# Performance work log

Hardware: AMD Instinct MI355X
Metric: run time of the kernel (lower is better)

## Reference

```python
import jax, jax.numpy as jnp
import numpy as np

NODES = 23   # 22 players + ball per frame-graph
K = 8        # random neighbors per node
B, T = 64, 128
G = B * T            # total graphs (frames)
N = G * NODES        # total nodes
D_IN, H, RH = 16, 128, 128


def setup_inputs() -> dict:
    key = jax.random.key(0)
    ks = jax.random.split(key, 10)
    x = jax.random.normal(ks[0], (N, D_IN), jnp.float32)
    # per-graph random edges: dst = each node repeated K times, src = random node in same graph
    src_local = jax.random.randint(ks[1], (G, NODES * K), 0, NODES)
    dst_local = jnp.tile(jnp.repeat(jnp.arange(NODES), K)[None, :], (G, 1))
    off = (jnp.arange(G) * NODES)[:, None]
    edge_index = jnp.stack([(src_local + off).reshape(-1),
                            (dst_local + off).reshape(-1)]).astype(jnp.int32)
    runner_idx = jax.random.randint(ks[2], (G,), 0, NODES, dtype=jnp.int32)
    sc = lambda k, sh: (jax.random.normal(k, sh, jnp.float32) * 0.05)
    return {
        'x': x, 'edge_index': edge_index, 'runner_idx': runner_idx,
        'W1': sc(ks[3], (D_IN, H)), 'b1': jnp.zeros((H,), jnp.float32),
        'W2': sc(ks[4], (H, H)),    'b2': jnp.zeros((H,), jnp.float32),
        'W_ih': sc(ks[5], (3 * RH, H)), 'W_hh': sc(ks[6], (3 * RH, RH)),
        'b_ih': jnp.zeros((3 * RH,), jnp.float32), 'b_hh': jnp.zeros((3 * RH,), jnp.float32),
        'Wp': sc(ks[7], (RH, 2)), 'bp': jnp.zeros((2,), jnp.float32),
    }


def _gcn_conv(h, edge_index, W, b):
    # PyG GCNConv: add self-loops, symmetric normalization, scatter-sum
    h = h @ W
    loop = jnp.arange(N, dtype=edge_index.dtype)
    s = jnp.concatenate([edge_index[0], loop])
    d = jnp.concatenate([edge_index[1], loop])
    deg = jax.ops.segment_sum(jnp.ones_like(s, h.dtype), d, num_segments=N)
    dinv = jnp.where(deg > 0, jax.lax.rsqrt(deg), 0.0)
    norm = dinv[s] * dinv[d]                      # [E+N]
    out = jax.ops.segment_sum(h[s] * norm[:, None], d, num_segments=N)
    return out + b


def _gru(seq, W_ih, W_hh, b_ih, b_hh):
    # torch GRU: gates in r,z,n order
    xg = seq @ W_ih.T + b_ih                      # [B,T,3RH]
    def step(hprev, xt):
        gh = hprev @ W_hh.T + b_hh
        xr, xz, xn = jnp.split(xt, 3, axis=-1)
        hr, hz, hn = jnp.split(gh, 3, axis=-1)
        r = jax.nn.sigmoid(xr + hr)
        z = jax.nn.sigmoid(xz + hz)
        n = jnp.tanh(xn + r * hn)
        hnew = (1.0 - z) * n + z * hprev
        return hnew, hnew
    h0 = jnp.zeros((seq.shape[0], RH), seq.dtype)
    _, outs = jax.lax.scan(step, h0, jnp.swapaxes(xg, 0, 1))
    return jnp.swapaxes(outs, 0, 1)               # [B,T,RH]


def reference(x, edge_index, runner_idx, W1, b1, W2, b2,
              W_ih, W_hh, b_ih, b_hh, Wp, bp):
    h = jax.nn.relu(_gcn_conv(x, edge_index, W1, b1))
    h = jax.nn.relu(_gcn_conv(h, edge_index, W2, b2))
    # fused equivalent of the per-graph nonzero()/indexing loop:
    runner_global = jnp.arange(G, dtype=jnp.int32) * NODES + runner_idx
    seq = h[runner_global].reshape(B, T, H)       # all lengths == T, padding is a no-op
    out = _gru(seq, W_ih, W_hh, b_ih, b_hh)
    return out @ Wp + bp                          # [B,T,2]
```

## Files before the change

### kernel.cpp

```cpp
#include <hip/hip_runtime.h>
#include <hip/hip_bf16.h>
#include <math.h>

#define GG 8192
#define NODESN 23
#define KK 8
#define DIN 16
#define HH 128
#define RHH 128
#define EPG (NODESN*KK)
#define TTT 128
#define BBB 64

template<int CTRL>
static __device__ __forceinline__ float dpp_add(float v) {
    int x = __builtin_amdgcn_update_dpp(0, __float_as_int(v), CTRL, 0xF, 0xF, true);
    return v + __int_as_float(x);
}
#define DPP_XOR1 0xB1
#define DPP_XOR2 0x4E
#define DPP_SHL4 0x104

__global__ __launch_bounds__(256) void gcn_hsum(
    const float* __restrict__ x, const int* __restrict__ esrc,
    const int* __restrict__ runner,
    const float* __restrict__ W1, const float* __restrict__ b1,
    float* __restrict__ xg )
{
    __shared__ float xs[NODESN * DIN];
    __shared__ int   srcs[EPG];
    __shared__ float t1[NODESN * HH];
    __shared__ float red[256];

    const int g   = blockIdx.x;
    const int tid = threadIdx.x;
    const int j   = tid & 127;
    const int nh  = tid >> 7;

    for (int i = tid; i < NODESN * DIN; i += 256) xs[i] = x[g * NODESN * DIN + i];
    for (int i = tid; i < EPG; i += 256)          srcs[i] = esrc[g * EPG + i] - g * NODESN;

    float w[DIN];
    #pragma unroll
    for (int k = 0; k < DIN; k++) w[k] = W1[k * HH + j];
    const float b1j = b1[j];
    __syncthreads();

    const int n0 = nh * 12;
    const int n1 = nh ? NODESN : 12;
    for (int n = n0; n < n1; n++) {
        float acc = 0.f;
        #pragma unroll
        for (int k = 0; k < DIN; k += 4) {
            float4 xv = *(const float4*)&xs[n * DIN + k];
            acc = fmaf(xv.x, w[k], fmaf(xv.y, w[k+1], fmaf(xv.z, w[k+2], fmaf(xv.w, w[k+3], acc))));
        }
        t1[n * HH + j] = acc;
    }
    __syncthreads();

    const int r = runner[g];
    float part = 0.f;
    for (int slot = nh; slot < 9; slot += 2) {
        int node = (slot < 8) ? srcs[r * KK + slot] : r;
        float acc = t1[node * HH + j];
        #pragma unroll
        for (int k = 0; k < KK; k++) acc += t1[srcs[node * KK + k] * HH + j];
        part += fmaxf(acc * (1.f / 9.f) + b1j, 0.f);
    }
    red[tid] = part;
    __syncthreads();
    if (tid < HH) xg[(size_t)g * 384 + tid] = red[tid] + red[tid + 128];
}

__global__ void pack_wih(const float* __restrict__ W, float* __restrict__ WTp)
{
    int idx = blockIdx.x * 256 + threadIdx.x;
    if (idx < 3 * RHH * RHH) {
        int j = idx / RHH, k = idx - j * RHH;
        WTp[(k >> 2) * (384 * 4) + j * 4 + (k & 3)] = W[idx];
    }
}

__global__ __launch_bounds__(384) void seqxg_kernel(
    float* __restrict__ xg, const float* __restrict__ W2,
    const float* __restrict__ b2, const float* __restrict__ WTp,
    const float* __restrict__ b_ih)
{
    __shared__ float hsb[16 * HH];
    __shared__ float sqb[16 * HH];
    const int tid = threadIdx.x;
    const size_t row0 = (size_t)blockIdx.x * 16;

    for (int v = tid; v < 16 * 32; v += 384) {
        int m = v >> 5, e = v & 31;
        ((float4*)hsb)[m * 32 + e] = *(const float4*)&xg[(row0 + m) * 384 + e * 4];
    }
    __syncthreads();

    {
        const int j = tid & 127, m0 = tid >> 7;
        const int nm = (m0 == 0) ? 6 : 5;
        float acc[6];
        #pragma unroll
        for (int t = 0; t < 6; t++) acc[t] = 0.f;
        for (int k = 0; k < HH; k += 4) {
            float w0 = W2[(k+0)*HH + j];
            float w1 = W2[(k+1)*HH + j];
            float w2 = W2[(k+2)*HH + j];
            float w3 = W2[(k+3)*HH + j];
            #pragma unroll
            for (int t = 0; t < 6; t++) {
                if (t < nm) {
                    float4 hv = *(const float4*)&hsb[(m0 + 3*t) * HH + k];
                    acc[t] = fmaf(hv.x, w0, fmaf(hv.y, w1, fmaf(hv.z, w2, fmaf(hv.w, w3, acc[t]))));
                }
            }
        }
        const float bj = b2[j];
        for (int t = 0; t < nm; t++)
            sqb[(m0 + 3*t) * HH + j] = fmaxf(acc[t] * (1.f/9.f) + bj, 0.f);
    }
    __syncthreads();

    {
        const int j2 = tid;
        float acc[16];
        const float bv = b_ih[j2];
        #pragma unroll
        for (int m = 0; m < 16; m++) acc[m] = bv;
        for (int k4 = 0; k4 < 32; k4++) {
            float4 wv = *(const float4*)&WTp[k4 * (384*4) + j2 * 4];
            #pragma unroll
            for (int m = 0; m < 16; m++) {
                float4 hv = *(const float4*)&sqb[m * HH + k4 * 4];
                acc[m] = fmaf(hv.x, wv.x, fmaf(hv.y, wv.y, fmaf(hv.z, wv.z, fmaf(hv.w, wv.w, acc[m]))));
            }
        }
        #pragma unroll
        for (int m = 0; m < 16; m++)
            xg[(row0 + m) * 384 + j2] = acc[m];
    }
}

#define CHUNK 32
#define NCH (TTT / CHUNK)
#define HPAD 132
#define XGB_FLOATS (CHUNK * HH * 4)

__global__ __launch_bounds__(512)
__attribute__((amdgpu_waves_per_eu(2, 2)))
void gru_kernel(
    const float* __restrict__ xg, const float* __restrict__ W_hh,
    const float* __restrict__ b_hh, const float* __restrict__ Wp,
    const float* __restrict__ bp, float* __restrict__ out)
{
    __shared__ float xgbuf[XGB_FLOATS];
    __shared__ float houtb[(CHUNK + 2) * HPAD];
    __shared__ float wps[2 * RHH + 2];

    const int b   = blockIdx.x;
    const int tid = threadIdx.x;
    const int q   = tid & 7;
    const int g   = tid >> 3;
    const int i0  = 2 * g, i1 = 2 * g + 1;

    float4 wr0[4], wz0[4], wn0[4], wr1[4], wz1[4], wn1[4];
    int lof[4];
    {
        const float* r0 = W_hh + (size_t)i0 * RHH;
        const float* z0 = r0 + (size_t)RHH * RHH;
        const float* n0 = z0 + (size_t)RHH * RHH;
        const float* r1 = W_hh + (size_t)i1 * RHH;
        const float* z1 = r1 + (size_t)RHH * RHH;
        const float* n1 = z1 + (size_t)RHH * RHH;
        #pragma unroll
        for (int m = 0; m < 4; m++) {
            int o = q * 16 + 4 * ((m + q) & 3);
            lof[m] = o;
            wr0[m] = *(const float4*)(r0 + o);
            wz0[m] = *(const float4*)(z0 + o);
            wn0[m] = *(const float4*)(n0 + o);
            wr1[m] = *(const float4*)(r1 + o);
            wz1[m] = *(const float4*)(z1 + o);
            wn1[m] = *(const float4*)(n1 + o);
        }
    }
    const float bhr0 = b_hh[i0], bhz0 = b_hh[RHH + i0], bhn0 = b_hh[2 * RHH + i0];
    const float bhr1 = b_hh[i1], bhz1 = b_hh[RHH + i1], bhn1 = b_hh[2 * RHH + i1];

    if (tid < 2 * RHH) wps[tid] = Wp[tid];
    if (tid < 2)       wps[2 * RHH + tid] = bp[tid];
    if (tid < HH)      houtb[CHUNK * HPAD + tid] = 0.f;
    float hp0 = 0.f, hp1 = 0.f;

    const float* xbase = xg + (size_t)b * TTT * 3 * RHH;
    float* outb = out + (size_t)b * TTT * 2;

    float pxr[8], pxz[8], pxn[8];
    #pragma unroll
    for (int k = 0; k < 8; k++) {
        int slot = tid + (k << 9);
        int tl = slot >> 7, ii = slot & 127;
        const float* p = xbase + (size_t)tl * 384 + ii;
        pxr[k] = p[0]; pxz[k] = p[128]; pxn[k] = p[256];
    }
    __syncthreads();

    for (int c = 0; c < NCH; c++) {
        #pragma unroll
        for (int k = 0; k < 8; k++) {
            int slot = tid + (k << 9);
            int tl = slot >> 7, ii = slot & 127;
            float4 v; v.x = pxr[k]; v.y = pxz[k]; v.z = pxn[k]; v.w = 0.f;
            *(float4*)&xgbuf[(tl << 9) + (ii << 2)] = v;
        }
        if (c + 1 < NCH) {
            #pragma unroll
            for (int k = 0; k < 8; k++) {
                int slot = tid + (k << 9);
                int tl = slot >> 7, ii = slot & 127;
                const float* p = xbase + (size_t)((c + 1) * CHUNK + tl) * 384 + ii;
                pxr[k] = p[0]; pxz[k] = p[128]; pxn[k] = p[256];
            }
        }
        if (c > 0) {
            const int s  = tid & 7;
            const int cc = (tid >> 3) & 1;
            const int tl = tid >> 4;
            const float* hr = &houtb[(tl + 1) * HPAD + s * 16];
            float acc = 0.f;
            #pragma unroll
            for (int jj = 0; jj < 4; jj++) {
                int mm = ((jj + s) & 3) << 2;
                float4 hv = *(const float4*)(hr + mm);
                int k = s * 16 + mm;
                acc = fmaf(hv.x, wps[(k+0)*2 + cc],
                      fmaf(hv.y, wps[(k+1)*2 + cc],
                      fmaf(hv.z, wps[(k+2)*2 + cc],
                      fmaf(hv.w, wps[(k+3)*2 + cc], acc))));
            }
            acc = dpp_add<DPP_XOR1>(acc);
            acc = dpp_add<DPP_XOR2>(acc);
            acc = dpp_add<DPP_SHL4>(acc);
            if (s == 0)
                outb[((c - 1) * CHUNK + tl) * 2 + cc] = acc + wps[2 * RHH + cc];
        }
        __syncthreads();

        for (int tl = 0; tl < CHUNK; tl++) {
            const float* hrow = &houtb[(tl == 0 ? CHUNK : tl) * HPAD];
            float ar0 = 0.f, az0 = 0.f, an0 = 0.f, ar1 = 0.f, az1 = 0.f, an1 = 0.f;
            #pragma unroll
            for (int m = 0; m < 4; m++) {
                float4 hv = *(const float4*)(hrow + lof[m]);
                ar0 = fmaf(hv.x, wr0[m].x, fmaf(hv.y, wr0[m].y, fmaf(hv.z, wr0[m].z, fmaf(hv.w, wr0[m].w, ar0))));
                az0 = fmaf(hv.x, wz0[m].x, fmaf(hv.y, wz0[m].y, fmaf(hv.z, wz0[m].z, fmaf(hv.w, wz0[m].w, az0))));
                an0 = fmaf(hv.x, wn0[m].x, fmaf(hv.y, wn0[m].y, fmaf(hv.z, wn0[m].z, fmaf(hv.w, wn0[m].w, an0))));
                ar1 = fmaf(hv.x, wr1[m].x, fmaf(hv.y, wr1[m].y, fmaf(hv.z, wr1[m].z, fmaf(hv.w, wr1[m].w, ar1))));
                az1 = fmaf(hv.x, wz1[m].x, fmaf(hv.y, wz1[m].y, fmaf(hv.z, wz1[m].z, fmaf(hv.w, wz1[m].w, az1))));
                an1 = fmaf(hv.x, wn1[m].x, fmaf(hv.y, wn1[m].y, fmaf(hv.z, wn1[m].z, fmaf(hv.w, wn1[m].w, an1))));
            }
            float4 x0 = *(const float4*)&xgbuf[(tl << 9) + (i0 << 2)];
            float4 x1 = *(const float4*)&xgbuf[(tl << 9) + (i1 << 2)];

            ar0 = dpp_add<DPP_XOR1>(ar0); ar0 = dpp_add<DPP_XOR2>(ar0); ar0 = dpp_add<DPP_SHL4>(ar0);
            az0 = dpp_add<DPP_XOR1>(az0); az0 = dpp_add<DPP_XOR2>(az0); az0 = dpp_add<DPP_SHL4>(az0);
            an0 = dpp_add<DPP_XOR1>(an0); an0 = dpp_add<DPP_XOR2>(an0); an0 = dpp_add<DPP_SHL4>(an0);
            ar1 = dpp_add<DPP_XOR1>(ar1); ar1 = dpp_add<DPP_XOR2>(ar1); ar1 = dpp_add<DPP_SHL4>(ar1);
            az1 = dpp_add<DPP_XOR1>(az1); az1 = dpp_add<DPP_XOR2>(az1); az1 = dpp_add<DPP_SHL4>(az1);
            an1 = dpp_add<DPP_XOR1>(an1); an1 = dpp_add<DPP_XOR2>(an1); an1 = dpp_add<DPP_SHL4>(an1);

            {
                float sr = x0.x + ar0 + bhr0;
                float sz = x0.y + az0 + bhz0;
                float rg = 1.f / (1.f + __expf(-sr));
                float zg = 1.f / (1.f + __expf(-sz));
                float tv = fmaf(rg, an0 + bhn0, x0.z);
                tv = fminf(fmaxf(tv, -15.f), 15.f);
                float e2 = __expf(-2.f * tv);
                float ng = (1.f - e2) / (1.f + e2);
                hp0 = fmaf(zg, hp0, (1.f - zg) * ng);
            }
            {
                float sr = x1.x + ar1 + bhr1;
                float sz = x1.y + az1 + bhz1;
                float rg = 1.f / (1.f + __expf(-sr));
                float zg = 1.f / (1.f + __expf(-sz));
                float tv = fmaf(rg, an1 + bhn1, x1.z);
                tv = fminf(fmaxf(tv, -15.f), 15.f);
                float e2 = __expf(-2.f * tv);
                float ng = (1.f - e2) / (1.f + e2);
                hp1 = fmaf(zg, hp1, (1.f - zg) * ng);
            }
            if (q == 0) {
                float2 hw; hw.x = hp0; hw.y = hp1;
                *(float2*)&houtb[(tl + 1) * HPAD + i0] = hw;
            }
            __syncthreads();
        }
    }

    {
        const int s  = tid & 7;
        const int cc = (tid >> 3) & 1;
        const int tl = tid >> 4;
        const float* hr = &houtb[(tl + 1) * HPAD + s * 16];
        float acc = 0.f;
        #pragma unroll
        for (int jj = 0; jj < 4; jj++) {
            int mm = ((jj + s) & 3) << 2;
            float4 hv = *(const float4*)(hr + mm);
            int k = s * 16 + mm;
            acc = fmaf(hv.x, wps[(k+0)*2 + cc],
                  fmaf(hv.y, wps[(k+1)*2 + cc],
                  fmaf(hv.z, wps[(k+2)*2 + cc],
                  fmaf(hv.w, wps[(k+3)*2 + cc], acc))));
        }
        acc = dpp_add<DPP_XOR1>(acc);
        acc = dpp_add<DPP_XOR2>(acc);
        acc = dpp_add<DPP_SHL4>(acc);
        if (s == 0)
            outb[((NCH - 1) * CHUNK + tl) * 2 + cc] = acc + wps[2 * RHH + cc];
    }
}

extern "C" void kernel_launch(void* const* d_in, const int* in_sizes, int n_in,
                              void* d_out, int out_size, void* d_ws, size_t ws_size,
                              hipStream_t stream)
{
    const float* x      = (const float*)d_in[0];
    const int*   eidx   = (const int*)d_in[1];
    const int*   runner = (const int*)d_in[2];
    const float* W1     = (const float*)d_in[3];
    const float* b1     = (const float*)d_in[4];
    const float* W2     = (const float*)d_in[5];
    const float* b2     = (const float*)d_in[6];
    const float* W_ih   = (const float*)d_in[7];
    const float* W_hh   = (const float*)d_in[8];
    const float* b_ih   = (const float*)d_in[9];
    const float* b_hh   = (const float*)d_in[10];
    const float* Wp     = (const float*)d_in[11];
    const float* bp     = (const float*)d_in[12];
    float* out = (float*)d_out;

    float* xg  = (float*)d_ws;
    float* WTp = xg + (size_t)GG * 3 * RHH;

    pack_wih<<<192, 256, 0, stream>>>(W_ih, WTp);
    gcn_hsum<<<GG, 256, 0, stream>>>(x, eidx, runner, W1, b1, xg);
    seqxg_kernel<<<GG / 16, 384, 0, stream>>>(xg, W2, b2, WTp, b_ih);
    gru_kernel<<<BBB, 512, 0, stream>>>(xg, W_hh, b_hh, Wp, bp, out);
}
```

Baseline: 256.9 us.

## Restructure GRU recurrence to one hidden unit per 4-lane group with packed FMA

The GRU kernel now assigns one hidden unit to each group of 4 lanes, where before it assigned two units to each group of 8. Each lane holds 96 weights as float2 vectors, so the matvec can use packed dual-FMA and needs only two DPP reduction steps instead of three. The register prefetch of the next xg chunk is dropped, so each chunk is loaded from global memory directly before the barrier. This adds global load latency on the serial path, and the wider per-lane weight set raises register pressure.

```diff
diff --git a/kernel.cpp b/kernel.cpp
--- a/kernel.cpp
+++ b/kernel.cpp
@@ -12,6 +12,8 @@
 #define TTT 128
 #define BBB 64
 
+typedef float v2f __attribute__((ext_vector_type(2)));
+
 template<int CTRL>
 static __device__ __forceinline__ float dpp_add(float v) {
     int x = __builtin_amdgcn_update_dpp(0, __float_as_int(v), CTRL, 0xF, 0xF, true);
@@ -19,13 +21,12 @@
 }
 #define DPP_XOR1 0xB1
 #define DPP_XOR2 0x4E
-#define DPP_SHL4 0x104
 
 __global__ __launch_bounds__(256) void gcn_hsum(
     const float* __restrict__ x, const int* __restrict__ esrc,
     const int* __restrict__ runner,
     const float* __restrict__ W1, const float* __restrict__ b1,
-    float* __restrict__ xg )
+    float* __restrict__ xg)
 {
     __shared__ float xs[NODESN * DIN];
     __shared__ int   srcs[EPG];
@@ -156,85 +157,135 @@
     const float* __restrict__ bp, float* __restrict__ out)
 {
     __shared__ float xgbuf[XGB_FLOATS];
-    __shared__ float houtb[(CHUNK + 2) * HPAD];
+    __shared__ float houtb[(CHUNK + 1) * HPAD];
     __shared__ float wps[2 * RHH + 2];
 
     const int b   = blockIdx.x;
     const int tid = threadIdx.x;
-    const int q   = tid & 7;
-    const int g   = tid >> 3;
-    const int i0  = 2 * g, i1 = 2 * g + 1;
-
-    float4 wr0[4], wz0[4], wn0[4], wr1[4], wz1[4], wn1[4];
-    int lof[4];
+    const int q   = tid & 3;
+    const int i   = tid >> 2;
+
+    v2f wr2[16], wz2[16], wn2[16];
+    int lof[8];
     {
-        const float* r0 = W_hh + (size_t)i0 * RHH;
-        const float* z0 = r0 + (size_t)RHH * RHH;
-        const float* n0 = z0 + (size_t)RHH * RHH;
-        const float* r1 = W_hh + (size_t)i1 * RHH;
-        const float* z1 = r1 + (size_t)RHH * RHH;
-        const float* n1 = z1 + (size_t)RHH * RHH;
-        #pragma unroll
-        for (int m = 0; m < 4; m++) {
-            int o = q * 16 + 4 * ((m + q) & 3);
-            lof[m] = o;
-            wr0[m] = *(const float4*)(r0 + o);
-            wz0[m] = *(const float4*)(z0 + o);
-            wn0[m] = *(const float4*)(n0 + o);
-            wr1[m] = *(const float4*)(r1 + o);
-            wz1[m] = *(const float4*)(z1 + o);
-            wn1[m] = *(const float4*)(n1 + o);
-        }
-    }
-    const float bhr0 = b_hh[i0], bhz0 = b_hh[RHH + i0], bhn0 = b_hh[2 * RHH + i0];
-    const float bhr1 = b_hh[i1], bhz1 = b_hh[RHH + i1], bhn1 = b_hh[2 * RHH + i1];
+        const float* br = W_hh + (size_t)i * RHH + q * 32;
+        const float* bz = br + (size_t)RHH * RHH;
+        const float* bn = bz + (size_t)RHH * RHH;
+        #pragma unroll
+        for (int m = 0; m < 8; m++) {
+            int p = (m + 2 * q) & 7;
+            lof[m] = q * 32 + 4 * p;
+            float4 v;
+            v = *(const float4*)(br + 4*p); wr2[2*m] = (v2f){v.x, v.y}; wr2[2*m+1] = (v2f){v.z, v.w};
+            v = *(const float4*)(bz + 4*p); wz2[2*m] = (v2f){v.x, v.y}; wz2[2*m+1] = (v2f){v.z, v.w};
+            v = *(const float4*)(bn + 4*p); wn2[2*m] = (v2f){v.x, v.y}; wn2[2*m+1] = (v2f){v.z, v.w};
+        }
+    }
+    const float bhr = b_hh[i];
+    const float bhz = b_hh[RHH + i];
+    const float bhn = b_hh[2 * RHH + i];
 
     if (tid < 2 * RHH) wps[tid] = Wp[tid];
     if (tid < 2)       wps[2 * RHH + tid] = bp[tid];
-    if (tid < HH)      houtb[CHUNK * HPAD + tid] = 0.f;
-    float hp0 = 0.f, hp1 = 0.f;
+    if (tid < HH)      houtb[tid] = 0.f;
+    float hprev = 0.f;
 
     const float* xbase = xg + (size_t)b * TTT * 3 * RHH;
     float* outb = out + (size_t)b * TTT * 2;
 
-    float pxr[8], pxz[8], pxn[8];
-    #pragma unroll
-    for (int k = 0; k < 8; k++) {
-        int slot = tid + (k << 9);
-        int tl = slot >> 7, ii = slot & 127;
-        const float* p = xbase + (size_t)tl * 384 + ii;
-        pxr[k] = p[0]; pxz[k] = p[128]; pxn[k] = p[256];
-    }
-    __syncthreads();
-
     for (int c = 0; c < NCH; c++) {
         #pragma unroll
-        for (int k = 0; k < 8; k++) {
-            int slot = tid + (k << 9);
+        for (int k2 = 0; k2 < 8; k2++) {
+            int slot = tid + (k2 << 9);
             int tl = slot >> 7, ii = slot & 127;
-            float4 v; v.x = pxr[k]; v.y = pxz[k]; v.z = pxn[k]; v.w = 0.f;
-            *(float4*)&xgbuf[(tl << 9) + (ii << 2)] = v;
-        }
-        if (c + 1 < NCH) {
+            const float* gsrc = xbase + (size_t)(c * CHUNK + tl) * 384 + ii;
+            float4 v;
+            v.x = gsrc[0]; v.y = gsrc[128]; v.z = gsrc[256]; v.w = 0.f;
+            *(float4*)&xgbuf[slot << 2] = v;
+        }
+        if (c > 0) {
+            const int s  = tid & 3;
+            const int cc = (tid >> 2) & 1;
+            const int tl = tid >> 3;
+            if (tl < CHUNK) {
+                const float* hr = &houtb[(tl + 1) * HPAD + s * 32];
+                float acc = 0.f;
+                #pragma unroll
+                for (int jj = 0; jj < 8; jj++) {
+                    int mm = 4 * ((jj + 2 * s) & 7);
+                    float4 hv = *(const float4*)(hr + mm);
+                    int k = s * 32 + mm;
+                    acc = fmaf(hv.x, wps[(k+0)*2 + cc],
+                          fmaf(hv.y, wps[(k+1)*2 + cc],
+                          fmaf(hv.z, wps[(k+2)*2 + cc],
+                          fmaf(hv.w, wps[(k+3)*2 + cc], acc))));
+                }
+                acc = dpp_add<DPP_XOR1>(acc);
+                acc = dpp_add<DPP_XOR2>(acc);
+                if (s == 0)
+                    outb[((c - 1) * CHUNK + tl) * 2 + cc] = acc + wps[2 * RHH + cc];
+            }
+        }
+        __syncthreads();
+
+        for (int tl = 0; tl < CHUNK; tl++) {
+            const float* hrow = &houtb[tl * HPAD];
+            float4 xgv = *(const float4*)&xgbuf[(tl * HH + i) << 2];
+            v2f arA = (v2f){0.f, 0.f}, arB = arA, azA = arA, azB = arA, anA = arA, anB = arA;
             #pragma unroll
-            for (int k = 0; k < 8; k++) {
-                int slot = tid + (k << 9);
-                int tl = slot >> 7, ii = slot & 127;
-                const float* p = xbase + (size_t)((c + 1) * CHUNK + tl) * 384 + ii;
-                pxr[k] = p[0]; pxz[k] = p[128]; pxn[k] = p[256];
-            }
-        }
-        if (c > 0) {
-            const int s  = tid & 7;
-            const int cc = (tid >> 3) & 1;
-            const int tl = tid >> 4;
-            const float* hr = &houtb[(tl + 1) * HPAD + s * 16];
+            for (int m = 0; m < 8; m++) {
+                float4 hv = *(const float4*)(hrow + lof[m]);
+                v2f h0 = (v2f){hv.x, hv.y};
+                v2f h1 = (v2f){hv.z, hv.w};
+                if (m & 1) {
+                    arB = h0 * wr2[2*m] + arB; arB = h1 * wr2[2*m+1] + arB;
+                    azB = h0 * wz2[2*m] + azB; azB = h1 * wz2[2*m+1] + azB;
+                    anB = h0 * wn2[2*m] + anB; anB = h1 * wn2[2*m+1] + anB;
+                } else {
+                    arA = h0 * wr2[2*m] + arA; arA = h1 * wr2[2*m+1] + arA;
+                    azA = h0 * wz2[2*m] + azA; azA = h1 * wz2[2*m+1] + azA;
+                    anA = h0 * wn2[2*m] + anA; anA = h1 * wn2[2*m+1] + anA;
+                }
+            }
+            v2f arv = arA + arB, azv = azA + azB, anv = anA + anB;
+            float ar = arv.x + arv.y;
+            float az = azv.x + azv.y;
+            float an = anv.x + anv.y;
+
+            ar = dpp_add<DPP_XOR1>(ar); ar = dpp_add<DPP_XOR2>(ar);
+            az = dpp_add<DPP_XOR1>(az); az = dpp_add<DPP_XOR2>(az);
+            an = dpp_add<DPP_XOR1>(an); an = dpp_add<DPP_XOR2>(an);
+
+            {
+                float sr = xgv.x + ar + bhr;
+                float sz = xgv.y + az + bhz;
+                float rg = 1.f / (1.f + __expf(-sr));
+                float zg = 1.f / (1.f + __expf(-sz));
+                float tv = fmaf(rg, an + bhn, xgv.z);
+                tv = fminf(fmaxf(tv, -15.f), 15.f);
+                float e2 = __expf(-2.f * tv);
+                float ng = (1.f - e2) / (1.f + e2);
+                hprev = fmaf(zg, hprev, (1.f - zg) * ng);
+            }
+            if (q == 0) houtb[(tl + 1) * HPAD + i] = hprev;
+            __syncthreads();
+        }
+        if (q == 0) houtb[i] = hprev;
+        __syncthreads();
+    }
+
+    {
+        const int s  = tid & 3;
+        const int cc = (tid >> 2) & 1;
+        const int tl = tid >> 3;
+        if (tl < CHUNK) {
+            const float* hr = &houtb[(tl + 1) * HPAD + s * 32];
             float acc = 0.f;
             #pragma unroll
-            for (int jj = 0; jj < 4; jj++) {
-                int mm = ((jj + s) & 3) << 2;
+            for (int jj = 0; jj < 8; jj++) {
+                int mm = 4 * ((jj + 2 * s) & 7);
                 float4 hv = *(const float4*)(hr + mm);
-                int k = s * 16 + mm;
+                int k = s * 32 + mm;
                 acc = fmaf(hv.x, wps[(k+0)*2 + cc],
                       fmaf(hv.y, wps[(k+1)*2 + cc],
                       fmaf(hv.z, wps[(k+2)*2 + cc],
@@ -242,86 +293,9 @@
             }
             acc = dpp_add<DPP_XOR1>(acc);
             acc = dpp_add<DPP_XOR2>(acc);
-            acc = dpp_add<DPP_SHL4>(acc);
             if (s == 0)
-                outb[((c - 1) * CHUNK + tl) * 2 + cc] = acc + wps[2 * RHH + cc];
-        }
-        __syncthreads();
-
-        for (int tl = 0; tl < CHUNK; tl++) {
-            const float* hrow = &houtb[(tl == 0 ? CHUNK : tl) * HPAD];
-            float ar0 = 0.f, az0 = 0.f, an0 = 0.f, ar1 = 0.f, az1 = 0.f, an1 = 0.f;
-            #pragma unroll
-            for (int m = 0; m < 4; m++) {
-                float4 hv = *(const float4*)(hrow + lof[m]);
-                ar0 = fmaf(hv.x, wr0[m].x, fmaf(hv.y, wr0[m].y, fmaf(hv.z, wr0[m].z, fmaf(hv.w, wr0[m].w, ar0))));
-                az0 = fmaf(hv.x, wz0[m].x, fmaf(hv.y, wz0[m].y, fmaf(hv.z, wz0[m].z, fmaf(hv.w, wz0[m].w, az0))));
-                an0 = fmaf(hv.x, wn0[m].x, fmaf(hv.y, wn0[m].y, fmaf(hv.z, wn0[m].z, fmaf(hv.w, wn0[m].w, an0))));
-                ar1 = fmaf(hv.x, wr1[m].x, fmaf(hv.y, wr1[m].y, fmaf(hv.z, wr1[m].z, fmaf(hv.w, wr1[m].w, ar1))));
-                az1 = fmaf(hv.x, wz1[m].x, fmaf(hv.y, wz1[m].y, fmaf(hv.z, wz1[m].z, fmaf(hv.w, wz1[m].w, az1))));
-                an1 = fmaf(hv.x, wn1[m].x, fmaf(hv.y, wn1[m].y, fmaf(hv.z, wn1[m].z, fmaf(hv.w, wn1[m].w, an1))));
-            }
-            float4 x0 = *(const float4*)&xgbuf[(tl << 9) + (i0 << 2)];
-            float4 x1 = *(const float4*)&xgbuf[(tl << 9) + (i1 << 2)];
-
-            ar0 = dpp_add<DPP_XOR1>(ar0); ar0 = dpp_add<DPP_XOR2>(ar0); ar0 = dpp_add<DPP_SHL4>(ar0);
-            az0 = dpp_add<DPP_XOR1>(az0); az0 = dpp_add<DPP_XOR2>(az0); az0 = dpp_add<DPP_SHL4>(az0);
-            an0 = dpp_add<DPP_XOR1>(an0); an0 = dpp_add<DPP_XOR2>(an0); an0 = dpp_add<DPP_SHL4>(an0);
-            ar1 = dpp_add<DPP_XOR1>(ar1); ar1 = dpp_add<DPP_XOR2>(ar1); ar1 = dpp_add<DPP_SHL4>(ar1);
-            az1 = dpp_add<DPP_XOR1>(az1); az1 = dpp_add<DPP_XOR2>(az1); az1 = dpp_add<DPP_SHL4>(az1);
-            an1 = dpp_add<DPP_XOR1>(an1); an1 = dpp_add<DPP_XOR2>(an1); an1 = dpp_add<DPP_SHL4>(an1);
-
-            {
-                float sr = x0.x + ar0 + bhr0;
-                float sz = x0.y + az0 + bhz0;
-                float rg = 1.f / (1.f + __expf(-sr));
-                float zg = 1.f / (1.f + __expf(-sz));
-                float tv = fmaf(rg, an0 + bhn0, x0.z);
-                tv = fminf(fmaxf(tv, -15.f), 15.f);
-                float e2 = __expf(-2.f * tv);
-                float ng = (1.f - e2) / (1.f + e2);
-                hp0 = fmaf(zg, hp0, (1.f - zg) * ng);
-            }
-            {
-                float sr = x1.x + ar1 + bhr1;
-                float sz = x1.y + az1 + bhz1;
-                float rg = 1.f / (1.f + __expf(-sr));
-                float zg = 1.f / (1.f + __expf(-sz));
-                float tv = fmaf(rg, an1 + bhn1, x1.z);
-                tv = fminf(fmaxf(tv, -15.f), 15.f);
-                float e2 = __expf(-2.f * tv);
-                float ng = (1.f - e2) / (1.f + e2);
-                hp1 = fmaf(zg, hp1, (1.f - zg) * ng);
-            }
-            if (q == 0) {
-                float2 hw; hw.x = hp0; hw.y = hp1;
-                *(float2*)&houtb[(tl + 1) * HPAD + i0] = hw;
-            }
-            __syncthreads();
-        }
-    }
-
-    {
-        const int s  = tid & 7;
-        const int cc = (tid >> 3) & 1;
-        const int tl = tid >> 4;
-        const float* hr = &houtb[(tl + 1) * HPAD + s * 16];
-        float acc = 0.f;
-        #pragma unroll
-        for (int jj = 0; jj < 4; jj++) {
-            int mm = ((jj + s) & 3) << 2;
-            float4 hv = *(const float4*)(hr + mm);
-            int k = s * 16 + mm;
-            acc = fmaf(hv.x, wps[(k+0)*2 + cc],
-                  fmaf(hv.y, wps[(k+1)*2 + cc],
-                  fmaf(hv.z, wps[(k+2)*2 + cc],
-                  fmaf(hv.w, wps[(k+3)*2 + cc], acc))));
-        }
-        acc = dpp_add<DPP_XOR1>(acc);
-        acc = dpp_add<DPP_XOR2>(acc);
-        acc = dpp_add<DPP_SHL4>(acc);
-        if (s == 0)
-            outb[((NCH - 1) * CHUNK + tl) * 2 + cc] = acc + wps[2 * RHH + cc];
+                outb[((NCH - 1) * CHUNK + tl) * 2 + cc] = acc + wps[2 * RHH + cc];
+        }
     }
 }
 
```

Result: faster. 245.3 us (-4.5%).
